# Optimization experiments

Hardware: AMD Instinct MI355X
Metric: run time of the kernel (lower is better)

The kernel has to match this reference:

```python
import jax, jax.numpy as jnp
import numpy as np

TEMP1, TEMP2, TEMP3 = 4.0, 5.0, 10.0
NORM_EPS = 1e-12   # F.normalize eps
COS_EPS = 1e-8     # custom_cosine_similarity eps


def setup_inputs() -> dict:
    key = jax.random.key(0)
    k1, k2 = jax.random.split(key)
    vis_embeds = jax.random.normal(k1, (16, 16, 16, 16, 128), dtype=jnp.float32)
    txt_embeds = jax.random.normal(k2, (16, 64, 128), dtype=jnp.float32)
    return {"vis_embeds": vis_embeds, "txt_embeds": txt_embeds}


def reference(vis_embeds, txt_embeds):
    # vis_embeds: [bs, h, w, d, E]; txt_embeds: [bs, T, E] (uniform token_len)
    bs, h, w, d, E = vis_embeds.shape
    S = h * w * d
    # L2-normalize along embedding dim (F.normalize)
    vn = vis_embeds / jnp.clip(jnp.linalg.norm(vis_embeds, axis=-1, keepdims=True), NORM_EPS)
    vn = vn.reshape(bs, S, E)                      # context, flattened source
    tn = txt_embeds / jnp.clip(jnp.linalg.norm(txt_embeds, axis=-1, keepdims=True), NORM_EPS)
    # attention_fn, vectorized over the outer loop index i (txt sample):
    # attn0[i,b,s,t] = <context_b[s], query_i[t]>
    attn0 = jnp.einsum('bse,ite->ibst', vn, tn)    # [bs_txt, bs_vis, S, T]
    s1 = jax.nn.softmax(attn0, axis=-1)            # softmax over query tokens t
    a = jax.nn.softmax(TEMP1 * jnp.swapaxes(s1, -1, -2), axis=-1)  # [i,b,t,s], softmax over s
    # weighted context: [i,b,t,E]
    wc = jnp.einsum('ibts,bse->ibte', a, vn)
    # custom cosine similarity along E between txt tokens and weighted context
    num = jnp.einsum('ibte,ite->ibt', wc, tn)
    w1 = jnp.linalg.norm(tn, axis=-1)              # [i,t] (== 1 up to normalize eps)
    w2 = jnp.linalg.norm(wc, axis=-1)              # [i,b,t]
    cos = num / jnp.clip(w1[:, None, :] * w2, COS_EPS)
    # row_sim: mul temp2, exp, sum over tokens (agg='sum'), log
    row = jnp.log(jnp.sum(jnp.exp(TEMP2 * cos), axis=-1))  # [i_txt, b_vis]
    sims = row.T * TEMP3                           # [b_vis, i_txt] matches torch cat(dim=1)
    labels = jnp.arange(bs)
    logp0 = jax.nn.log_softmax(sims, axis=-1)
    logp1 = jax.nn.log_softmax(sims.T, axis=-1)
    loss0 = -jnp.mean(logp0[labels, labels])
    loss1 = -jnp.mean(logp1[labels, labels])
    loss = (loss0 + loss1) / 2.0
    # att_maps: for sample i the original keeps attn[i] -> diagonal of [i,b,...]
    att_maps = a[labels, labels].reshape(bs, -1, h, w, d)  # [bs, T, h, w, d]
    return loss, att_maps
```

## Files before the change

### kernel.cpp

```cpp
#include <hip/hip_runtime.h>

constexpr int BS = 16;
constexpr int S  = 4096;
constexpr int E  = 128;
constexpr int T  = 64;
constexpr int CH = 256;
constexpr int NCH = S / CH;
constexpr int ETS = 268;
constexpr int TNS = 136;
constexpr int PTS = 264;

constexpr long VN_OFF  = 0;
constexpr long VNT_OFF = (long)BS * S * E;
constexpr long WS_F    = (long)BS * S * E;

typedef __attribute__((ext_vector_type(8))) short bf16x8;
typedef __attribute__((ext_vector_type(4))) short bf16x4;
typedef __attribute__((ext_vector_type(4))) float f32x4;

__device__ __forceinline__ unsigned short f2bf(float x) {
    unsigned u = __float_as_uint(x);
    u += 0x7FFFu + ((u >> 16) & 1u);
    return (unsigned short)(u >> 16);
}
__device__ __forceinline__ float bf2f(unsigned short v) {
    return __uint_as_float(((unsigned)v) << 16);
}
__device__ __forceinline__ bf16x8 ld_b64x2(const unsigned short* p) {
    const bf16x4 lo = *(const bf16x4*)p;
    const bf16x4 hi = *(const bf16x4*)(p + 4);
    bf16x8 r;
    r[0]=lo[0]; r[1]=lo[1]; r[2]=lo[2]; r[3]=lo[3];
    r[4]=hi[0]; r[5]=hi[1]; r[6]=hi[2]; r[7]=hi[3];
    return r;
}

__global__ __launch_bounds__(1024, 4)
void prep_kernel(const float* __restrict__ vis, unsigned short* __restrict__ wsv)
{
    __shared__ unsigned short Lt[128 * PTS];
    const int tid  = threadIdx.x;
    const int b    = blockIdx.x >> 4;
    const int tile = blockIdx.x & 15;
    const int s0   = tile * 256;
    const float* visb = vis + ((long)b * S + s0) * E;
    unsigned short* vn  = wsv + VN_OFF  + ((long)b * S + s0) * E;
    unsigned short* vnT = wsv + VNT_OFF + (long)b * E * S;

    {
        const int pp = tid >> 3, ee = tid & 7;
        const float* rA = visb + (long)(pp << 1) * E + (ee << 1);
        float2 va[8], vb[8];
        float sa = 0.f, sb = 0.f;
#pragma unroll
        for (int k = 0; k < 8; ++k) {
            va[k] = *(const float2*)(rA + (k << 4));
            vb[k] = *(const float2*)(rA + E + (k << 4));
            sa = fmaf(va[k].x, va[k].x, fmaf(va[k].y, va[k].y, sa));
            sb = fmaf(vb[k].x, vb[k].x, fmaf(vb[k].y, vb[k].y, sb));
        }
        sa += __shfl_xor(sa, 1); sa += __shfl_xor(sa, 2); sa += __shfl_xor(sa, 4);
        sb += __shfl_xor(sb, 1); sb += __shfl_xor(sb, 2); sb += __shfl_xor(sb, 4);
        const float ia = 1.0f / fmaxf(sqrtf(sa), 1e-12f);
        const float ib = 1.0f / fmaxf(sqrtf(sb), 1e-12f);
        const long r0 = (long)(pp << 1) * E, r1 = r0 + E;
#pragma unroll
        for (int k = 0; k < 8; ++k) {
            const int e0 = (ee << 1) + (k << 4);
            const unsigned ax = f2bf(va[k].x * ia), ay = f2bf(va[k].y * ia);
            const unsigned bx = f2bf(vb[k].x * ib), by = f2bf(vb[k].y * ib);
            *(unsigned*)&Lt[e0 * PTS + (pp << 1)]       = ax | (bx << 16);
            *(unsigned*)&Lt[(e0 + 1) * PTS + (pp << 1)] = ay | (by << 16);
            *(unsigned*)&vn[r0 + e0] = ax | (ay << 16);
            *(unsigned*)&vn[r1 + e0] = bx | (by << 16);
        }
    }
    __syncthreads();
    {
        const int e = tid >> 3, sseg = (tid & 7) << 5;
#pragma unroll
        for (int k = 0; k < 4; ++k) {
            const bf16x8 v = *(const bf16x8*)&Lt[e * PTS + sseg + (k << 3)];
            *(bf16x8*)&vnT[(long)e * S + s0 + sseg + (k << 3)] = v;
        }
    }
}

__global__ __launch_bounds__(1024, 4)
void clip_main_kernel(const unsigned short* __restrict__ wsv,
                      const float* __restrict__ txt,
                      float* __restrict__ d_out,
                      float* __restrict__ wsf)
{
    __shared__ unsigned short ET[2][T * ETS];
    __shared__ unsigned short tnL[T * TNS];
    __shared__ float scrA[512], scrB[512];

    const int tid = threadIdx.x;
    const int w   = tid >> 6;
    const int l   = tid & 63;
    const int cl  = l & 15;
    const int q   = l >> 4;
    const int b   = blockIdx.x & 15;
    const int i   = blockIdx.x >> 4;
    const bool diag = (i == b);

    {
        const int r = tid >> 4, seg = tid & 15;
        const float* tp = txt + ((long)i * T + r) * E + (seg << 3);
        const float4 a0 = *(const float4*)(tp);
        const float4 a1 = *(const float4*)(tp + 4);
        float ssq = a0.x*a0.x + a0.y*a0.y + a0.z*a0.z + a0.w*a0.w
                  + a1.x*a1.x + a1.y*a1.y + a1.z*a1.z + a1.w*a1.w;
        ssq += __shfl_xor(ssq, 1); ssq += __shfl_xor(ssq, 2);
        ssq += __shfl_xor(ssq, 4); ssq += __shfl_xor(ssq, 8);
        const float inv = 1.0f / fmaxf(sqrtf(ssq), 1e-12f);
        bf16x8 f;
        f[0]=(short)f2bf(a0.x*inv); f[1]=(short)f2bf(a0.y*inv);
        f[2]=(short)f2bf(a0.z*inv); f[3]=(short)f2bf(a0.w*inv);
        f[4]=(short)f2bf(a1.x*inv); f[5]=(short)f2bf(a1.y*inv);
        f[6]=(short)f2bf(a1.z*inv); f[7]=(short)f2bf(a1.w*inv);
        *(bf16x8*)&tnL[r * TNS + (seg << 3)] = f;
    }
    __syncthreads();

    bf16x8 tA0[2][4];
#pragma unroll
    for (int mt = 0; mt < 2; ++mt)
#pragma unroll
        for (int kk = 0; kk < 4; ++kk)
            tA0[mt][kk] = *(const bf16x8*)&tnL[((mt << 4) + cl) * TNS + (kk << 5) + (q << 3)];

    f32x4 acc2[2];
    acc2[0] = (f32x4){0.f,0.f,0.f,0.f};
    acc2[1] = (f32x4){0.f,0.f,0.f,0.f};
    const int et  = w >> 1;
    const int ntb = (w & 1) << 1;

    const unsigned short* vnb  = wsv + VN_OFF  + (long)b * S * E;
    const unsigned short* vntb = wsv + VNT_OFF + (long)b * E * S;
    float* attb = d_out + 1 + (long)b * (long)T * S;

    for (int ch = 0; ch <= NCH; ++ch) {
        const int cb = ch & 1, pb = cb ^ 1;

        bf16x8 Bf[4];
        if (ch < NCH) {
            const unsigned short* r0 = vnb + (long)(ch * CH + (w << 4) + cl) * E + (q << 3);
#pragma unroll
            for (int kk = 0; kk < 4; ++kk) Bf[kk] = *(const bf16x8*)(r0 + (kk << 5));
        }

        if (ch > 0) {
            const int s0p = (ch - 1) * CH;
            const unsigned short* ar  = vntb + (long)((et << 4) + cl) * S + s0p + (q << 3);
            const unsigned short* e0p = &ET[pb][((ntb << 4) + cl) * ETS + (q << 3)];
            const unsigned short* e1p = e0p + (ETS << 4);
#pragma unroll
            for (int kk2 = 0; kk2 < 8; ++kk2) {
                const bf16x8 aV = *(const bf16x8*)(ar + (kk2 << 5));
                const bf16x8 b0 = ld_b64x2(e0p + (kk2 << 5));
                const bf16x8 b1 = ld_b64x2(e1p + (kk2 << 5));
                acc2[0] = __builtin_amdgcn_mfma_f32_16x16x32_bf16(aV, b0, acc2[0], 0, 0, 0);
                acc2[1] = __builtin_amdgcn_mfma_f32_16x16x32_bf16(aV, b1, acc2[1], 0, 0, 0);
            }
        }

        if (ch < NCH) {
            f32x4 acc1[4];
#pragma unroll
            for (int mt = 0; mt < 4; ++mt) acc1[mt] = (f32x4){0.f,0.f,0.f,0.f};
#pragma unroll
            for (int kk = 0; kk < 4; ++kk) {
                acc1[0] = __builtin_amdgcn_mfma_f32_16x16x32_bf16(tA0[0][kk], Bf[kk], acc1[0], 0, 0, 0);
                acc1[1] = __builtin_amdgcn_mfma_f32_16x16x32_bf16(tA0[1][kk], Bf[kk], acc1[1], 0, 0, 0);
                const bf16x8 t2 = *(const bf16x8*)&tnL[(32 + cl) * TNS + (kk << 5) + (q << 3)];
                const bf16x8 t3 = *(const bf16x8*)&tnL[(48 + cl) * TNS + (kk << 5) + (q << 3)];
                acc1[2] = __builtin_amdgcn_mfma_f32_16x16x32_bf16(t2, Bf[kk], acc1[2], 0, 0, 0);
                acc1[3] = __builtin_amdgcn_mfma_f32_16x16x32_bf16(t3, Bf[kk], acc1[3], 0, 0, 0);
            }
            float ex[4][4];
            float ssum = 0.f;
#pragma unroll
            for (int mt = 0; mt < 4; ++mt)
#pragma unroll
                for (int r = 0; r < 4; ++r) {
                    const float v = __expf(acc1[mt][r]);
                    ex[mt][r] = v; ssum += v;
                }
            ssum += __shfl_xor(ssum, 16);
            ssum += __shfl_xor(ssum, 32);
            const float csc = 4.0f / ssum;
            const int sloc = (w << 4) + cl;
#pragma unroll
            for (int mt = 0; mt < 4; ++mt)
#pragma unroll
                for (int r = 0; r < 4; ++r)
                    ET[cb][((mt << 4) + (q << 2) + r) * ETS + sloc] = f2bf(__expf(ex[mt][r] * csc));
        }

        if (diag && ch > 0) {
            const int s0p = (ch - 1) * CH;
            const int t = tid >> 4, sg = (tid & 15) << 4;
            float* ap = attb + (long)t * S + s0p + sg;
#pragma unroll
            for (int k = 0; k < 8; ++k) {
                const ushort2 v = *(const ushort2*)&ET[pb][t * ETS + sg + (k << 1)];
                ap[(k << 1) + 0] = bf2f(v.x);
                ap[(k << 1) + 1] = bf2f(v.y);
            }
        }

        if (ch < NCH) __syncthreads();
    }

    {
        float pn[2] = {0.f, 0.f}, pw[2] = {0.f, 0.f};
#pragma unroll
        for (int j = 0; j < 2; ++j) {
            const int t = ((ntb + j) << 4) + cl;
            const ushort4 tns = *(const ushort4*)&tnL[t * TNS + (et << 4) + (q << 2)];
            const float tv0 = bf2f(tns.x), tv1 = bf2f(tns.y), tv2 = bf2f(tns.z), tv3 = bf2f(tns.w);
            pn[j] = acc2[j][0]*tv0 + acc2[j][1]*tv1 + acc2[j][2]*tv2 + acc2[j][3]*tv3;
            pw[j] = acc2[j][0]*acc2[j][0] + acc2[j][1]*acc2[j][1]
                  + acc2[j][2]*acc2[j][2] + acc2[j][3]*acc2[j][3];
            pn[j] += __shfl_xor(pn[j], 16); pn[j] += __shfl_xor(pn[j], 32);
            pw[j] += __shfl_xor(pw[j], 16); pw[j] += __shfl_xor(pw[j], 32);
        }
        if (q == 0) {
#pragma unroll
            for (int j = 0; j < 2; ++j) {
                const int t = ((ntb + j) << 4) + cl;
                scrA[(et << 6) + t] = pn[j];
                scrB[(et << 6) + t] = pw[j];
            }
        }
        __syncthreads();
        if (tid < 64) {
            float num = 0.f, w2 = 0.f;
#pragma unroll
            for (int m = 0; m < 8; ++m) {
                num += scrA[(m << 6) + tid];
                w2  += scrB[(m << 6) + tid];
            }
            const float cosv = num / fmaxf(sqrtf(w2), 1e-20f);
            float r = __expf(5.0f * cosv);
#pragma unroll
            for (int m = 1; m < 64; m <<= 1) r += __shfl_xor(r, m);
            if (tid == 0) wsf[WS_F + (b << 4) + i] = 10.0f * logf(r);
        }
    }
}

__global__ __launch_bounds__(256, 4)
void att_norm_loss_kernel(float* __restrict__ d_out, const float* __restrict__ wsf)
{
    const int tid = threadIdx.x;
    if (blockIdx.x == BS * T) {
        __shared__ float sm[16][17];
        __shared__ float red[16];
        const int bb = tid >> 4, ii = tid & 15;
        const float x = wsf[WS_F + bb * 16 + ii];
        sm[bb][ii] = x;
        float m = x;
#pragma unroll
        for (int msk = 1; msk < 16; msk <<= 1) m = fmaxf(m, __shfl_xor(m, msk));
        float s = __expf(x - m);
#pragma unroll
        for (int msk = 1; msk < 16; msk <<= 1) s += __shfl_xor(s, msk);
        const float lsm0 = x - m - logf(s);
        __syncthreads();
        const float y = sm[ii][bb];
        float m1 = y;
#pragma unroll
        for (int msk = 1; msk < 16; msk <<= 1) m1 = fmaxf(m1, __shfl_xor(m1, msk));
        float s1 = __expf(y - m1);
#pragma unroll
        for (int msk = 1; msk < 16; msk <<= 1) s1 += __shfl_xor(s1, msk);
        const float lsm1 = y - m1 - logf(s1);
        if (bb == ii) red[bb] = lsm0 + lsm1;
        __syncthreads();
        if (tid == 0) {
            float tot = 0.f;
#pragma unroll
            for (int k = 0; k < 16; ++k) tot += red[k];
            d_out[0] = -tot / 32.0f;
        }
        return;
    }
    __shared__ float r4[4];
    const int bt = blockIdx.x;
    float* p = d_out + 1 + (long)bt * 4096;
    float v[16];
    float s = 0.f;
#pragma unroll
    for (int k = 0; k < 16; ++k) { v[k] = p[k * 256 + tid]; s += v[k]; }
#pragma unroll
    for (int m = 1; m < 64; m <<= 1) s += __shfl_xor(s, m);
    if ((tid & 63) == 0) r4[tid >> 6] = s;
    __syncthreads();
    const float inv = 1.0f / (r4[0] + r4[1] + r4[2] + r4[3]);
#pragma unroll
    for (int k = 0; k < 16; ++k) p[k * 256 + tid] = v[k] * inv;
}

extern "C" void kernel_launch(void* const* d_in, const int* in_sizes, int n_in,
                              void* d_out, int out_size, void* d_ws, size_t ws_size,
                              hipStream_t stream)
{
    const float* vis = (const float*)d_in[0];
    const float* txt = (const float*)d_in[1];
    float* out = (float*)d_out;
    unsigned short* wsv = (unsigned short*)d_ws;
    float* wsf = (float*)d_ws;

    hipLaunchKernelGGL(prep_kernel, dim3(256), dim3(1024), 0, stream, vis, wsv);
    hipLaunchKernelGGL(clip_main_kernel, dim3(BS * BS), dim3(1024), 0, stream,
                       wsv, txt, out, wsf);
    hipLaunchKernelGGL(att_norm_loss_kernel, dim3(BS * T + 1), dim3(256), 0, stream,
                       out, wsf);
}
```

Before: 221.3 us.

## Split sequence dimension across two blocks per pair and add a reduction kernel

The main kernel now launches two blocks per (txt, vis) pair, each covering half of the spatial positions. Each block writes its partial weighted-context accumulators to workspace, and a new reduce kernel sums the two halves and computes the cosine similarity and row similarity. The ET buffer is single-buffered with an extra barrier in place of the old double-buffered software pipeline. The intent is to fill the GPU with 512 blocks instead of 256. The cost is an extra launch, partial-sum traffic through global memory, and less overlap inside each block.

```diff
diff --git a/kernel.cpp b/kernel.cpp
--- a/kernel.cpp
+++ b/kernel.cpp
@@ -5,14 +5,17 @@
 constexpr int E  = 128;
 constexpr int T  = 64;
 constexpr int CH = 256;
-constexpr int NCH = S / CH;
-constexpr int ETS = 268;
+constexpr int NSP = 2;
+constexpr int SSEG = S / NSP;
+constexpr int NCH = SSEG / CH;
+constexpr int ETS = 260;
 constexpr int TNS = 136;
 constexpr int PTS = 264;
 
 constexpr long VN_OFF  = 0;
 constexpr long VNT_OFF = (long)BS * S * E;
-constexpr long WS_F    = (long)BS * S * E;
+constexpr long WS_P    = (long)BS * S * E;
+constexpr long WS_SIMS = WS_P + (long)256 * 2 * 8192;
 
 typedef __attribute__((ext_vector_type(8))) short bf16x8;
 typedef __attribute__((ext_vector_type(4))) short bf16x4;
@@ -86,23 +89,23 @@
     }
 }
 
-__global__ __launch_bounds__(1024, 4)
+__global__ __launch_bounds__(1024, 8)
 void clip_main_kernel(const unsigned short* __restrict__ wsv,
                       const float* __restrict__ txt,
                       float* __restrict__ d_out,
                       float* __restrict__ wsf)
 {
-    __shared__ unsigned short ET[2][T * ETS];
+    __shared__ unsigned short ET[T * ETS];
     __shared__ unsigned short tnL[T * TNS];
-    __shared__ float scrA[512], scrB[512];
-
-    const int tid = threadIdx.x;
-    const int w   = tid >> 6;
-    const int l   = tid & 63;
-    const int cl  = l & 15;
-    const int q   = l >> 4;
-    const int b   = blockIdx.x & 15;
-    const int i   = blockIdx.x >> 4;
+
+    const int tid  = threadIdx.x;
+    const int w    = tid >> 6;
+    const int l    = tid & 63;
+    const int cl   = l & 15;
+    const int q    = l >> 4;
+    const int b    = blockIdx.x & 15;
+    const int i    = (blockIdx.x >> 4) & 15;
+    const int half = blockIdx.x >> 8;
     const bool diag = (i == b);
 
     {
@@ -141,32 +144,17 @@
     const unsigned short* vntb = wsv + VNT_OFF + (long)b * E * S;
     float* attb = d_out + 1 + (long)b * (long)T * S;
 
-    for (int ch = 0; ch <= NCH; ++ch) {
-        const int cb = ch & 1, pb = cb ^ 1;
+    for (int ch = 0; ch < NCH; ++ch) {
+        const int s0 = half * SSEG + ch * CH;
 
         bf16x8 Bf[4];
-        if (ch < NCH) {
-            const unsigned short* r0 = vnb + (long)(ch * CH + (w << 4) + cl) * E + (q << 3);
+        {
+            const unsigned short* r0 = vnb + (long)(s0 + (w << 4) + cl) * E + (q << 3);
 #pragma unroll
             for (int kk = 0; kk < 4; ++kk) Bf[kk] = *(const bf16x8*)(r0 + (kk << 5));
         }
 
-        if (ch > 0) {
-            const int s0p = (ch - 1) * CH;
-            const unsigned short* ar  = vntb + (long)((et << 4) + cl) * S + s0p + (q << 3);
-            const unsigned short* e0p = &ET[pb][((ntb << 4) + cl) * ETS + (q << 3)];
-            const unsigned short* e1p = e0p + (ETS << 4);
-#pragma unroll
-            for (int kk2 = 0; kk2 < 8; ++kk2) {
-                const bf16x8 aV = *(const bf16x8*)(ar + (kk2 << 5));
-                const bf16x8 b0 = ld_b64x2(e0p + (kk2 << 5));
-                const bf16x8 b1 = ld_b64x2(e1p + (kk2 << 5));
-                acc2[0] = __builtin_amdgcn_mfma_f32_16x16x32_bf16(aV, b0, acc2[0], 0, 0, 0);
-                acc2[1] = __builtin_amdgcn_mfma_f32_16x16x32_bf16(aV, b1, acc2[1], 0, 0, 0);
-            }
-        }
-
-        if (ch < NCH) {
+        {
             f32x4 acc1[4];
 #pragma unroll
             for (int mt = 0; mt < 4; ++mt) acc1[mt] = (f32x4){0.f,0.f,0.f,0.f};
@@ -196,59 +184,82 @@
             for (int mt = 0; mt < 4; ++mt)
 #pragma unroll
                 for (int r = 0; r < 4; ++r)
-                    ET[cb][((mt << 4) + (q << 2) + r) * ETS + sloc] = f2bf(__expf(ex[mt][r] * csc));
-        }
-
-        if (diag && ch > 0) {
-            const int s0p = (ch - 1) * CH;
+                    ET[((mt << 4) + (q << 2) + r) * ETS + sloc] = f2bf(__expf(ex[mt][r] * csc));
+        }
+        __syncthreads();
+
+        {
+            const unsigned short* ar  = vntb + (long)((et << 4) + cl) * S + s0 + (q << 3);
+            const unsigned short* e0p = &ET[((ntb << 4) + cl) * ETS + (q << 3)];
+            const unsigned short* e1p = e0p + (ETS << 4);
+#pragma unroll
+            for (int kk2 = 0; kk2 < 8; ++kk2) {
+                const bf16x8 aV = *(const bf16x8*)(ar + (kk2 << 5));
+                const bf16x8 b0 = ld_b64x2(e0p + (kk2 << 5));
+                const bf16x8 b1 = ld_b64x2(e1p + (kk2 << 5));
+                acc2[0] = __builtin_amdgcn_mfma_f32_16x16x32_bf16(aV, b0, acc2[0], 0, 0, 0);
+                acc2[1] = __builtin_amdgcn_mfma_f32_16x16x32_bf16(aV, b1, acc2[1], 0, 0, 0);
+            }
+        }
+
+        if (diag) {
             const int t = tid >> 4, sg = (tid & 15) << 4;
-            float* ap = attb + (long)t * S + s0p + sg;
+            float* ap = attb + (long)t * S + s0 + sg;
 #pragma unroll
             for (int k = 0; k < 8; ++k) {
-                const ushort2 v = *(const ushort2*)&ET[pb][t * ETS + sg + (k << 1)];
+                const ushort2 v = *(const ushort2*)&ET[t * ETS + sg + (k << 1)];
                 ap[(k << 1) + 0] = bf2f(v.x);
                 ap[(k << 1) + 1] = bf2f(v.y);
             }
         }
-
-        if (ch < NCH) __syncthreads();
+        __syncthreads();
     }
 
     {
-        float pn[2] = {0.f, 0.f}, pw[2] = {0.f, 0.f};
-#pragma unroll
-        for (int j = 0; j < 2; ++j) {
-            const int t = ((ntb + j) << 4) + cl;
-            const ushort4 tns = *(const ushort4*)&tnL[t * TNS + (et << 4) + (q << 2)];
-            const float tv0 = bf2f(tns.x), tv1 = bf2f(tns.y), tv2 = bf2f(tns.z), tv3 = bf2f(tns.w);
-            pn[j] = acc2[j][0]*tv0 + acc2[j][1]*tv1 + acc2[j][2]*tv2 + acc2[j][3]*tv3;
-            pw[j] = acc2[j][0]*acc2[j][0] + acc2[j][1]*acc2[j][1]
-                  + acc2[j][2]*acc2[j][2] + acc2[j][3]*acc2[j][3];
-            pn[j] += __shfl_xor(pn[j], 16); pn[j] += __shfl_xor(pn[j], 32);
-            pw[j] += __shfl_xor(pw[j], 16); pw[j] += __shfl_xor(pw[j], 32);
-        }
-        if (q == 0) {
-#pragma unroll
-            for (int j = 0; j < 2; ++j) {
+        float* pp = wsf + WS_P + ((long)(((i << 4) + b) * 2 + half)) * 8192;
+#pragma unroll
+        for (int j = 0; j < 2; ++j)
+#pragma unroll
+            for (int r = 0; r < 4; ++r) {
+                const int e = (et << 4) + (q << 2) + r;
                 const int t = ((ntb + j) << 4) + cl;
-                scrA[(et << 6) + t] = pn[j];
-                scrB[(et << 6) + t] = pw[j];
+                pp[e * 64 + t] = acc2[j][r];
             }
-        }
-        __syncthreads();
-        if (tid < 64) {
-            float num = 0.f, w2 = 0.f;
-#pragma unroll
-            for (int m = 0; m < 8; ++m) {
-                num += scrA[(m << 6) + tid];
-                w2  += scrB[(m << 6) + tid];
-            }
-            const float cosv = num / fmaxf(sqrtf(w2), 1e-20f);
-            float r = __expf(5.0f * cosv);
-#pragma unroll
-            for (int m = 1; m < 64; m <<= 1) r += __shfl_xor(r, m);
-            if (tid == 0) wsf[WS_F + (b << 4) + i] = 10.0f * logf(r);
-        }
+    }
+}
+
+__global__ __launch_bounds__(256, 8)
+void reduce_kernel(const float* __restrict__ txt, float* __restrict__ wsf)
+{
+    __shared__ float sA[256], sB[256], sC[256];
+    const int tid = threadIdx.x;
+    const int t = tid & 63, w4 = tid >> 6;
+    const int pair = blockIdx.x;
+    const int i = pair >> 4, b = pair & 15;
+    const float* p0 = wsf + WS_P + (long)(pair * 2) * 8192;
+    const float* p1 = p0 + 8192;
+    const float* tp = txt + ((long)i * T + t) * E + (w4 << 5);
+
+    float ssq = 0.f, num = 0.f, w2 = 0.f;
+#pragma unroll 8
+    for (int e = 0; e < 32; ++e) {
+        const float tv = tp[e];
+        const float wc = p0[((w4 << 5) + e) * 64 + t] + p1[((w4 << 5) + e) * 64 + t];
+        ssq = fmaf(tv, tv, ssq);
+        num = fmaf(wc, tv, num);
+        w2  = fmaf(wc, wc, w2);
+    }
+    sA[tid] = ssq; sB[tid] = num; sC[tid] = w2;
+    __syncthreads();
+    if (tid < 64) {
+        const float ss = sA[tid] + sA[64 + tid] + sA[128 + tid] + sA[192 + tid];
+        const float nm = sB[tid] + sB[64 + tid] + sB[128 + tid] + sB[192 + tid];
+        const float ww = sC[tid] + sC[64 + tid] + sC[128 + tid] + sC[192 + tid];
+        const float cosv = (nm / fmaxf(sqrtf(ss), 1e-12f)) / fmaxf(sqrtf(ww), 1e-20f);
+        float r = __expf(5.0f * cosv);
+#pragma unroll
+        for (int m = 1; m < 64; m <<= 1) r += __shfl_xor(r, m);
+        if (tid == 0) wsf[WS_SIMS + (b << 4) + i] = 10.0f * logf(r);
     }
 }
 
@@ -260,7 +271,7 @@
         __shared__ float sm[16][17];
         __shared__ float red[16];
         const int bb = tid >> 4, ii = tid & 15;
-        const float x = wsf[WS_F + bb * 16 + ii];
+        const float x = wsf[WS_SIMS + bb * 16 + ii];
         sm[bb][ii] = x;
         float m = x;
 #pragma unroll
@@ -315,8 +326,9 @@
     float* wsf = (float*)d_ws;
 
     hipLaunchKernelGGL(prep_kernel, dim3(256), dim3(1024), 0, stream, vis, wsv);
-    hipLaunchKernelGGL(clip_main_kernel, dim3(BS * BS), dim3(1024), 0, stream,
+    hipLaunchKernelGGL(clip_main_kernel, dim3(BS * BS * NSP), dim3(1024), 0, stream,
                        wsv, txt, out, wsf);
+    hipLaunchKernelGGL(reduce_kernel, dim3(BS * BS), dim3(256), 0, stream, txt, wsf);
     hipLaunchKernelGGL(att_norm_loss_kernel, dim3(BS * T + 1), dim3(256), 0, stream,
                        out, wsf);
 }
```

Result: slower. 269.1 us (+21.6%).
